# Optimization experiments

Hardware: AMD Instinct MI355X
Metric: run time of the kernel (lower is better)

The kernel has to match this reference:

```python
import jax, jax.numpy as jnp
import numpy as np

BN_EPS = 1e-5


def _tconv(X, w1, b1, w2, b2, w3, b3):
    # X: (B, T, N, C) -> conv over time with kernel (1, k), gated GLU-style
    Xp = X.transpose(0, 2, 1, 3)  # (B, N, T, C)
    def conv(w, b):
        return jax.lax.conv_general_dilated(
            Xp, w, (1, 1), 'VALID',
            dimension_numbers=('NHWC', 'HWIO', 'NHWC')) + b
    P = conv(w1, b1)
    Q = jax.nn.sigmoid(conv(w2, b2))
    R = conv(w3, b3)
    H = jax.nn.relu(P * Q + R)
    return H.transpose(0, 2, 1, 3)  # (B, T-k+1, N, Cout)


def _cheb(x, ei, W, b):
    # Batched ChebConv (sym norm, lambda_max=2 => L_hat = -D^-1/2 A D^-1/2)
    # x: (S, N, F), ei: (S, 2, E), W: (K, F, Fout)
    S, N, F = x.shape
    row, col = ei[:, 0], ei[:, 1]           # (S, E)
    ones = jnp.ones(ei.shape[-1], x.dtype)
    def norm_one(r, c):
        deg = jax.ops.segment_sum(ones, r, num_segments=N)
        dis = jnp.where(deg > 0, jax.lax.rsqrt(jnp.maximum(deg, 1.)), 0.)
        return -dis[r] * dis[c]
    w = jax.vmap(norm_one)(row, col)        # (S, E), constant wrt floats
    def prop(xs, r, c, ws):
        return jax.ops.segment_sum(ws[:, None] * xs[c], r, num_segments=N)
    propv = jax.vmap(prop)
    Tx = [x, propv(x, row, col, w)]
    for _ in range(W.shape[0] - 2):
        Tx.append(2. * propv(Tx[-1], row, col, w) - Tx[-2])
    return jnp.einsum('ksnf,kfo->sno', jnp.stack(Tx), W) + b


def _forward(X, tc1_w1, tc1_b1, tc1_w2, tc1_b2, tc1_w3, tc1_b3,
             cheb_w, cheb_b,
             tc2_w1, tc2_b1, tc2_w2, tc2_b2, tc2_w3, tc2_b3,
             bn_gamma, bn_beta, conv3_w, conv3_b, f1_w, f1_b, edge_index):
    T0 = _tconv(X, tc1_w1, tc1_b1, tc1_w2, tc1_b2, tc1_w3, tc1_b3)  # (B,38,N,H)
    B, Tt, N, H = T0.shape
    ei = edge_index[:, :Tt].reshape(B * Tt, 2, edge_index.shape[-1])
    G = _cheb(T0.reshape(B * Tt, N, H), ei, cheb_w, cheb_b)
    G = jax.nn.relu(G.reshape(B, Tt, N, H))
    T2 = _tconv(G, tc2_w1, tc2_b1, tc2_w2, tc2_b2, tc2_w3, tc2_b3)  # (B,36,N,Co)
    # BatchNorm2d over channel dim = num_nodes (training-mode batch stats)
    Tn = T2.transpose(0, 2, 1, 3)  # (B, N, T, C)
    mean = Tn.mean(axis=(0, 2, 3), keepdims=True)
    var = Tn.var(axis=(0, 2, 3), keepdims=True)
    Tn = (Tn - mean) * jax.lax.rsqrt(var + BN_EPS)
    Tn = Tn * bn_gamma[None, :, None, None] + bn_beta[None, :, None, None]
    Tb = Tn.transpose(0, 2, 1, 3)                 # (B, T, N, C)
    Tr = Tb.reshape(B, Tb.shape[1], -1)           # (B, T, N*C=3200)
    y = jax.lax.conv_general_dilated(
        Tr[:, None, :, :], conv3_w, (1, 1), 'VALID',
        dimension_numbers=('NCHW', 'OIHW', 'NCHW'))  # (B,128,T-2,1)
    y = y + conv3_b[None, :, None, None]
    y = y[:, :, :, 0]
    pooled = y.mean(axis=2)                        # AvgPool1d over full length
    return pooled @ f1_w + f1_b                    # (B, 3200)


def setup_inputs() -> dict:
    key = jax.random.key(0)
    ks = jax.random.split(key, 20)
    B, Tw, N, Cin, H, Co, E = 32, 40, 50, 2, 128, 64, 800
    KT, K = 3, 3
    s = 0.05
    d = {
        'X': jax.random.normal(ks[0], (B, Tw, N, Cin), jnp.float32),
        'edge_index': jax.random.randint(ks[1], (B, Tw, 2, E), 0, N),
        'tc1_w1': jax.random.normal(ks[2], (1, KT, Cin, H), jnp.float32) * s,
        'tc1_b1': jnp.zeros((H,), jnp.float32),
        'tc1_w2': jax.random.normal(ks[3], (1, KT, Cin, H), jnp.float32) * s,
        'tc1_b2': jnp.zeros((H,), jnp.float32),
        'tc1_w3': jax.random.normal(ks[4], (1, KT, Cin, H), jnp.float32) * s,
        'tc1_b3': jnp.zeros((H,), jnp.float32),
        'cheb_w': jax.random.normal(ks[5], (K, H, H), jnp.float32) * s,
        'cheb_b': jnp.zeros((H,), jnp.float32),
        'tc2_w1': jax.random.normal(ks[6], (1, KT, H, Co), jnp.float32) * s,
        'tc2_b1': jnp.zeros((Co,), jnp.float32),
        'tc2_w2': jax.random.normal(ks[7], (1, KT, H, Co), jnp.float32) * s,
        'tc2_b2': jnp.zeros((Co,), jnp.float32),
        'tc2_w3': jax.random.normal(ks[8], (1, KT, H, Co), jnp.float32) * s,
        'tc2_b3': jnp.zeros((Co,), jnp.float32),
        'bn_gamma': jnp.ones((N,), jnp.float32),
        'bn_beta': jnp.zeros((N,), jnp.float32),
        'conv3_w': jax.random.normal(ks[9], (128, 1, 3, N * Co), jnp.float32) * 0.01,
        'conv3_b': jnp.zeros((128,), jnp.float32),
        'f1_w': jax.random.normal(ks[10], (128, N * Co), jnp.float32) * s,
        'f1_b': jnp.zeros((N * Co,), jnp.float32),
    }
    return d


def reference(X, tc1_w1, tc1_b1, tc1_w2, tc1_b2, tc1_w3, tc1_b3,
              cheb_w, cheb_b,
              tc2_w1, tc2_b1, tc2_w2, tc2_b2, tc2_w3, tc2_b3,
              bn_gamma, bn_beta, conv3_w, conv3_b, f1_w, f1_b, edge_index):
    return _forward(X, tc1_w1, tc1_b1, tc1_w2, tc1_b2, tc1_w3, tc1_b3,
                    cheb_w, cheb_b,
                    tc2_w1, tc2_b1, tc2_w2, tc2_b2, tc2_w3, tc2_b3,
                    bn_gamma, bn_beta, conv3_w, conv3_b, f1_w, f1_b, edge_index)
```

## Files before the change

kernel.cpp:

```cpp
#include <hip/hip_runtime.h>
#include <hip/hip_bf16.h>

#define BB 32
#define TW 40
#define NN 50
#define HH 128
#define CO 64
#define EE 800
#define TT 38
#define TT2 36
#define TPOOL 34
#define NCO 3200
#define SS (BB*TT)
#define NPAD 64
#define RPAD (SS*NPAD)

#define PB_US ((size_t)RPAD * HH)
#define PB_BYTES (PB_US * 2)

typedef __attribute__((ext_vector_type(8))) short s16x8;
typedef __attribute__((ext_vector_type(16))) float f32x16;
typedef unsigned short us;

static __device__ __forceinline__ unsigned int f2bf_u(float x) {
    unsigned int u = __float_as_uint(x);
    return (u + 0x7fffu + ((u >> 16) & 1u)) >> 16;
}
static __device__ __forceinline__ float bfu2f(unsigned int h) {
    return __uint_as_float(h << 16);
}
static __device__ __forceinline__ size_t fragoff32(int m, int c) {
    return (size_t)(c >> 4) * 512 + ((c >> 3) & 1) * 256 + m * 8 + (c & 7);
}
#define MFMA(a, b, c) __builtin_amdgcn_mfma_f32_32x32x16_bf16((a), (b), (c), 0, 0, 0)

__global__ __launch_bounds__(256) void k_wprep(
    const float* __restrict__ cw,
    const float* __restrict__ tw1, const float* __restrict__ tw2, const float* __restrict__ tw3,
    us* __restrict__ VTh, us* __restrict__ VTl,
    us* __restrict__ WTh, us* __restrict__ WTl,
    float* __restrict__ pooled)
{
    int idx = blockIdx.x * 256 + threadIdx.x;
    float v; us *dh, *dl; int col, k;
    if (idx < 128 * 384) {
        col = idx / 384; k = idx % 384;
        if (k < 128)      v = cw[k * 128 + col] - cw[32768 + k * 128 + col];
        else if (k < 256) v = cw[16384 + (k - 128) * 128 + col];
        else              v = 2.f * cw[32768 + (k - 256) * 128 + col];
        dh = VTh; dl = VTl;
    } else if (idx < 128 * 384 + 192 * 384) {
        int i2 = idx - 128 * 384;
        col = i2 / 384; k = i2 % 384;
        int gg = col >> 6, o = col & 63;
        const float* src = (gg == 0) ? tw1 : (gg == 1) ? tw2 : tw3;
        v = src[k * 64 + o];
        dh = WTh; dl = WTl;
    } else {
        int z = idx - (128 * 384 + 192 * 384);
        if (z < 4096) pooled[z] = 0.f;
        return;
    }
    size_t off = ((size_t)((col >> 5) * 24 + (k >> 4)) * 64 + ((k >> 3) & 1) * 32 + (col & 31)) * 8
               + (k & 7);
    unsigned int h = f2bf_u(v);
    dh[off] = (us)h;
    dl[off] = (us)f2bf_u(v - bfu2f(h));
}

#define TAS 136
#define TBS 72
#define LMS 53
__global__ __launch_bounds__(256) void k_cheb(
    const int* __restrict__ EI, const float* __restrict__ X,
    const float* __restrict__ w1, const float* __restrict__ b1,
    const float* __restrict__ w2, const float* __restrict__ b2,
    const float* __restrict__ w3, const float* __restrict__ b3,
    const us* __restrict__ VTh, const us* __restrict__ VTl,
    const float* __restrict__ bias,
    us* __restrict__ Gh)
{
    __shared__ __align__(16) char smem[61440];
    us* TbA = (us*)smem;
    us* TbB = (us*)(smem + 17408);
    us* Pa  = (us*)(smem + 35840);
    float* Lm = (float*)(smem + 35840);
    us* LA  = (us*)(smem + 53248);
    float* Xs = (float*)(smem + 53248);
    int* deg  = (int*)(smem + 53248 + 1216);
    float* dis = (float*)(smem + 53248 + 1216 + 224);

    int g = blockIdx.x;
    int tid = threadIdx.x;
    int b = g / TT, t = g % TT;
    const int* row = EI + (size_t)(b * TW + t) * 2 * EE;
    const int* col = row + EE;

    {
        s16x8 zz = {0, 0, 0, 0, 0, 0, 0, 0};
        for (int i = tid; i < 2240; i += 256) ((s16x8*)smem)[i] = zz;
    }
    for (int i = tid; i < 52 * LMS; i += 256) Lm[i] = 0.f;
    for (int i = tid; i < 300; i += 256) Xs[i] = X[(size_t)(b * TW + t) * 100 + i];
    if (tid < NN) deg[tid] = 0;
    __syncthreads();

    {
        int c = tid & 127, nh = tid >> 7;
        float wr1[6], wr2[6], wr3[6];
#pragma unroll
        for (int q = 0; q < 6; q++) {
            wr1[q] = w1[q * HH + c];
            wr2[q] = w2[q * HH + c];
            wr3[q] = w3[q * HH + c];
        }
        float bv1 = b1[c], bv2 = b2[c], bv3 = b3[c];
        for (int n = nh; n < NN; n += 2) {
            float P = bv1, Q = bv2, R = bv3;
#pragma unroll
            for (int q = 0; q < 6; q++) {
                float x = Xs[(q >> 1) * 100 + n * 2 + (q & 1)];
                P += x * wr1[q]; Q += x * wr2[q]; R += x * wr3[q];
            }
            float sg = 1.f / (1.f + expf(-Q));
            float v = P * sg + R;
            v = v > 0.f ? v : 0.f;
            us h = (us)f2bf_u(v);
            TbA[n * TAS + c] = h;
            TbB[c * TBS + n] = h;
        }
    }
    __syncthreads();
    for (int e = tid; e < EE; e += 256) atomicAdd(&deg[row[e]], 1);
    __syncthreads();
    if (tid < NN) dis[tid] = deg[tid] > 0 ? rsqrtf((float)deg[tid]) : 0.f;
    __syncthreads();
    for (int e = tid; e < EE; e += 256) {
        int r = row[e], cc = col[e];
        atomicAdd(&Lm[r * LMS + cc], -dis[r] * dis[cc]);
    }
    __syncthreads();
    for (int ent = tid; ent < 512; ent += 256) {
        int lanee = ent & 63;
        int ks = (ent >> 6) & 3;
        int mt = ent >> 8;
        int m = mt * 32 + (lanee & 31);
        int kb = ks * 16 + (lanee >> 5) * 8;
        s16x8 v;
#pragma unroll
        for (int j = 0; j < 8; j++) {
            int k = kb + j;
            float lv = (m < NN && k < NN) ? Lm[m * LMS + k] : 0.f;
            v[j] = (short)f2bf_u(lv);
        }
        *(s16x8*)(LA + ent * 8) = v;
    }
    __syncthreads();

    int lane = tid & 63;
    int w = tid >> 6;
    int rg = w >> 1, fh = w & 1;
    int nl = lane & 31;
    int khalf = lane >> 5;
    size_t laneoff = (size_t)lane * 8;

    const us* vh0 = VTh + (size_t)(fh * 2) * 12288 + laneoff;
    const us* vh1 = VTh + (size_t)(fh * 2 + 1) * 12288 + laneoff;
    const us* vl0 = VTl + (size_t)(fh * 2) * 12288 + laneoff;
    const us* vl1 = VTl + (size_t)(fh * 2 + 1) * 12288 + laneoff;

    int mrowA = rg * 32 + nl;
    int kbb = khalf * 8;

    f32x16 gacc0, gacc1, d0, d1;
#pragma unroll
    for (int r = 0; r < 16; r++) { gacc0[r] = 0.f; gacc1[r] = 0.f; d0[r] = 0.f; d1[r] = 0.f; }

#pragma unroll
    for (int ks = 0; ks < 4; ks++) {
        s16x8 afr = *(const s16x8*)(LA + ((rg * 4 + ks) * 64 + lane) * 8);
        int kb = ks * 16 + kbb;
        s16x8 bf0 = *(const s16x8*)(TbB + (fh * 64 + nl) * TBS + kb);
        s16x8 bf1 = *(const s16x8*)(TbB + (fh * 64 + 32 + nl) * TBS + kb);
        d0 = MFMA(afr, bf0, d0);
        d1 = MFMA(afr, bf1, d1);
    }
#pragma unroll
    for (int ks = 0; ks < 8; ks++) {
        s16x8 ah = *(const s16x8*)(TbA + mrowA * TAS + ks * 16 + kbb);
        s16x8 bh0 = *(const s16x8*)(vh0 + ks * 512);
        s16x8 bl0 = *(const s16x8*)(vl0 + ks * 512);
        s16x8 bh1 = *(const s16x8*)(vh1 + ks * 512);
        s16x8 bl1 = *(const s16x8*)(vl1 + ks * 512);
        gacc0 = MFMA(ah, bh0, gacc0); gacc0 = MFMA(ah, bl0, gacc0);
        gacc1 = MFMA(ah, bh1, gacc1); gacc1 = MFMA(ah, bl1, gacc1);
    }
    __syncthreads();
#pragma unroll
    for (int r = 0; r < 16; r++) {
        int mrow = (r & 3) + 8 * (r >> 2) + 4 * khalf;
        int node = rg * 32 + mrow;
        int f0 = fh * 64 + nl, f1 = f0 + 32;
        us h0 = (us)f2bf_u(d0[r]);
        us h1 = (us)f2bf_u(d1[r]);
        Pa[node * TAS + f0] = h0;
        Pa[node * TAS + f1] = h1;
        TbB[f0 * TBS + node] = h0;
        TbB[f1 * TBS + node] = h1;
    }
    __syncthreads();

#pragma unroll
    for (int r = 0; r < 16; r++) { d0[r] = 0.f; d1[r] = 0.f; }
#pragma unroll
    for (int ks = 0; ks < 4; ks++) {
        s16x8 afr = *(const s16x8*)(LA + ((rg * 4 + ks) * 64 + lane) * 8);
        int kb = ks * 16 + kbb;
        s16x8 bf0 = *(const s16x8*)(TbB + (fh * 64 + nl) * TBS + kb);
        s16x8 bf1 = *(const s16x8*)(TbB + (fh * 64 + 32 + nl) * TBS + kb);
        d0 = MFMA(afr, bf0, d0);
        d1 = MFMA(afr, bf1, d1);
    }
#pragma unroll
    for (int ks = 0; ks < 8; ks++) {
        s16x8 ah = *(const s16x8*)(Pa + mrowA * TAS + ks * 16 + kbb);
        s16x8 bh0 = *(const s16x8*)(vh0 + (8 + ks) * 512);
        s16x8 bl0 = *(const s16x8*)(vl0 + (8 + ks) * 512);
        s16x8 bh1 = *(const s16x8*)(vh1 + (8 + ks) * 512);
        s16x8 bl1 = *(const s16x8*)(vl1 + (8 + ks) * 512);
        gacc0 = MFMA(ah, bh0, gacc0); gacc0 = MFMA(ah, bl0, gacc0);
        gacc1 = MFMA(ah, bh1, gacc1); gacc1 = MFMA(ah, bl1, gacc1);
    }
    __syncthreads();
#pragma unroll
    for (int r = 0; r < 16; r++) {
        int mrow = (r & 3) + 8 * (r >> 2) + 4 * khalf;
        int node = rg * 32 + mrow;
        int f0 = fh * 64 + nl, f1 = f0 + 32;
        Pa[node * TAS + f0] = (us)f2bf_u(d0[r]);
        Pa[node * TAS + f1] = (us)f2bf_u(d1[r]);
    }
    __syncthreads();
#pragma unroll
    for (int ks = 0; ks < 8; ks++) {
        s16x8 ah = *(const s16x8*)(Pa + mrowA * TAS + ks * 16 + kbb);
        s16x8 bh0 = *(const s16x8*)(vh0 + (16 + ks) * 512);
        s16x8 bl0 = *(const s16x8*)(vl0 + (16 + ks) * 512);
        s16x8 bh1 = *(const s16x8*)(vh1 + (16 + ks) * 512);
        s16x8 bl1 = *(const s16x8*)(vl1 + (16 + ks) * 512);
        gacc0 = MFMA(ah, bh0, gacc0); gacc0 = MFMA(ah, bl0, gacc0);
        gacc1 = MFMA(ah, bh1, gacc1); gacc1 = MFMA(ah, bl1, gacc1);
    }

    int c0 = fh * 64 + nl, c1 = c0 + 32;
    float bv0 = bias[c0], bv1 = bias[c1];
    size_t gb = (size_t)g * 8192 + (size_t)rg * 4096;
#pragma unroll
    for (int r = 0; r < 16; r++) {
        int mrow = (r & 3) + 8 * (r >> 2) + 4 * khalf;
        float v0 = gacc0[r] + bv0; v0 = v0 > 0.f ? v0 : 0.f;
        float v1 = gacc1[r] + bv1; v1 = v1 > 0.f ? v1 : 0.f;
        Gh[gb + fragoff32(mrow, c0)] = (us)f2bf_u(v0);
        Gh[gb + fragoff32(mrow, c1)] = (us)f2bf_u(v1);
    }
}

__global__ __launch_bounds__(128) void k_tc2(
    const us* __restrict__ Gh,
    const us* __restrict__ WTh, const us* __restrict__ WTl,
    const float* __restrict__ tb1, const float* __restrict__ tb2, const float* __restrict__ tb3,
    us* __restrict__ T2)
{
    int tid = threadIdx.x;
    int lane = tid & 63;
    int w = tid >> 6;
    int nl = lane & 31;
    size_t laneoff = (size_t)lane * 8;
    int i = blockIdx.x;
    int vb = (i & 7) * 288 + (i >> 3);
    int bt36 = vb >> 1, ntile = vb & 1;
    int b = bt36 / TT2, t = bt36 % TT2;

    const us* A[3];
#pragma unroll
    for (int k3 = 0; k3 < 3; k3++)
        A[k3] = Gh + (size_t)(b * TT + t + k3) * 8192 + (size_t)ntile * 4096 + laneoff;
    const us* Bh[3];
    const us* Bl[3];
#pragma unroll
    for (int g3 = 0; g3 < 3; g3++) {
        size_t cb = (size_t)(g3 * 2 + w) * 12288 + laneoff;
        Bh[g3] = WTh + cb;
        Bl[g3] = WTl + cb;
    }

    f32x16 aP, aQ, aR;
#pragma unroll
    for (int r = 0; r < 16; r++) { aP[r] = 0.f; aQ[r] = 0.f; aR[r] = 0.f; }

#pragma unroll
    for (int k3 = 0; k3 < 3; k3++) {
#pragma unroll
        for (int ls = 0; ls < 8; ls++) {
            int offB = (k3 * 8 + ls) * 512;
            s16x8 a0 = *(const s16x8*)(A[k3] + ls * 512);
            s16x8 ph = *(const s16x8*)(Bh[0] + offB);
            s16x8 pl = *(const s16x8*)(Bl[0] + offB);
            s16x8 qh = *(const s16x8*)(Bh[1] + offB);
            s16x8 ql = *(const s16x8*)(Bl[1] + offB);
            s16x8 rh = *(const s16x8*)(Bh[2] + offB);
            s16x8 rl = *(const s16x8*)(Bl[2] + offB);
            aP = MFMA(a0, ph, aP); aP = MFMA(a0, pl, aP);
            aQ = MFMA(a0, qh, aQ); aQ = MFMA(a0, ql, aQ);
            aR = MFMA(a0, rh, aR); aR = MFMA(a0, rl, aR);
        }
    }

    int o = w * 32 + nl;
    float bP = tb1[o], bQ = tb2[o], bR = tb3[o];
    int rbase = (lane >> 5) * 4;
#pragma unroll
    for (int r = 0; r < 16; r++) {
        int m = (r & 3) + 8 * (r >> 2) + rbase;
        int node = ntile * 32 + m;
        if (node < NN) {
            float P = aP[r] + bP, Q = aQ[r] + bQ, R = aR[r] + bR;
            float sg = 1.f / (1.f + expf(-Q));
            float v = P * sg + R;
            v = v > 0.f ? v : 0.f;
            T2[((size_t)bt36 * NN + node) * CO + o] = (us)f2bf_u(v);
        }
    }
}

__global__ __launch_bounds__(256) void k_bnpart(const us* __restrict__ T2, float* __restrict__ partial)
{
    int n = blockIdx.x >> 3, c = blockIdx.x & 7;
    int tid = threadIdx.x;
    float s = 0.f, ss = 0.f;
    for (int i = tid; i < 144 * 64; i += 256) {
        int bt = c * 144 + (i >> 6), o = i & 63;
        float v = bfu2f(T2[((size_t)bt * NN + n) * CO + o]);
        s += v; ss += v * v;
    }
    for (int off = 32; off > 0; off >>= 1) { s += __shfl_down(s, off, 64); ss += __shfl_down(ss, off, 64); }
    __shared__ float rs[4], rss[4];
    int lane = tid & 63, wv = tid >> 6;
    if (lane == 0) { rs[wv] = s; rss[wv] = ss; }
    __syncthreads();
    if (tid == 0) {
        partial[n * 8 + c] = rs[0] + rs[1] + rs[2] + rs[3];
        partial[400 + n * 8 + c] = rss[0] + rss[1] + rss[2] + rss[3];
    }
}

__global__ __launch_bounds__(64) void k_bnfin(const float* __restrict__ partial, float* __restrict__ stats)
{
    int n = threadIdx.x;
    if (n < NN) {
        float s = 0.f, ss = 0.f;
#pragma unroll
        for (int c = 0; c < 8; c++) { s += partial[n * 8 + c]; ss += partial[400 + n * 8 + c]; }
        const float inv = 1.f / (float)(BB * TT2 * CO);
        float m = s * inv;
        float var = ss * inv - m * m;
        stats[n] = m;
        stats[64 + n] = rsqrtf(var + 1e-5f);
    }
}

__global__ __launch_bounds__(256) void k_upool(
    const us* __restrict__ T2, const float* __restrict__ stats,
    const float* __restrict__ gamma, const float* __restrict__ beta,
    const float* __restrict__ W3, float* __restrict__ pooled)
{
    __shared__ __align__(16) float Ul[48 * 36 + 32];
    __shared__ float Ws[128 * 9];
    int blk = blockIdx.x;
    int jc = blk * 16;
    int n0 = jc >> 6;
    int tid = threadIdx.x;
    float mn = stats[n0], is = stats[64 + n0];
    float sc = is * gamma[n0];
    float off = (float)TPOOL * beta[n0] - (float)TPOOL * mn * sc;

    {
        int j = tid & 15, b0 = tid >> 4;
#pragma unroll
        for (int bp = 0; bp < 2; bp++) {
            int bb = b0 + 16 * bp;
            const us* p = T2 + (size_t)bb * TT2 * NCO + jc + j;
            float s0 = 0.f;
            for (int t = 0; t < TPOOL; t++) s0 += bfu2f(p[(size_t)t * NCO]);
            float s1 = s0 - bfu2f(p[0]) + bfu2f(p[(size_t)34 * NCO]);
            float s2 = s1 - bfu2f(p[(size_t)1 * NCO]) + bfu2f(p[(size_t)35 * NCO]);
            Ul[(0 * 16 + j) * 36 + bb] = s0 * sc + off;
            Ul[(1 * 16 + j) * 36 + bb] = s1 * sc + off;
            Ul[(2 * 16 + j) * 36 + bb] = s2 * sc + off;
        }
    }
    __syncthreads();

    int o = tid & 127, bq = tid >> 7;
    float acc[16];
#pragma unroll
    for (int i = 0; i < 16; i++) acc[i] = 0.f;

    for (int kjc = 0; kjc < 48; kjc += 8) {
        __syncthreads();
#pragma unroll
        for (int p4 = 0; p4 < 4; p4++) {
            int idx = p4 * 256 + tid;
            int oo = idx >> 3, q = idx & 7;
            int kj = kjc + q;
            Ws[oo * 9 + q] = W3[(size_t)oo * 9600 + (kj >> 4) * 3200 + jc + (kj & 15)];
        }
        __syncthreads();
#pragma unroll
        for (int q = 0; q < 8; q++) {
            float wv = Ws[o * 9 + q];
            const float* up = &Ul[(kjc + q) * 36 + bq * 16];
#pragma unroll
            for (int i4 = 0; i4 < 4; i4++) {
                float4 u = *(const float4*)(up + i4 * 4);
                acc[i4 * 4 + 0] += wv * u.x;
                acc[i4 * 4 + 1] += wv * u.y;
                acc[i4 * 4 + 2] += wv * u.z;
                acc[i4 * 4 + 3] += wv * u.w;
            }
        }
    }
#pragma unroll
    for (int i = 0; i < 16; i++)
        atomicAdd(&pooled[(size_t)(bq * 16 + i) * 128 + o], acc[i]);
}

__global__ __launch_bounds__(256) void k_final(
    const float* __restrict__ pooled, const float* __restrict__ b3c,
    const float* __restrict__ f1w, const float* __restrict__ f1b,
    float* __restrict__ out)
{
    __shared__ float pb[32 * 129];
    int tid = threadIdx.x;
    const float inv = 1.f / (float)TPOOL;
    for (int i = tid; i < 4096; i += 256) {
        int b = i >> 7, o = i & 127;
        pb[b * 129 + o] = pooled[b * 128 + o] * inv + b3c[o];
    }
    __syncthreads();
    int q = blockIdx.x * 8 + (tid & 7);
    int b = tid >> 3;
    float acc = f1b[q];
    const float* wq = f1w + q;
    const float* pbb = pb + b * 129;
#pragma unroll 4
    for (int o = 0; o < 128; o++) acc += pbb[o] * wq[(size_t)o * NCO];
    out[(size_t)b * NCO + q] = acc;
}

extern "C" void kernel_launch(void* const* d_in, const int* in_sizes, int n_in,
                              void* d_out, int out_size, void* d_ws, size_t ws_size,
                              hipStream_t stream)
{
    const float* X       = (const float*)d_in[0];
    const int*   EI      = (const int*)d_in[1];
    const float* tc1_w1  = (const float*)d_in[2];
    const float* tc1_b1  = (const float*)d_in[3];
    const float* tc1_w2  = (const float*)d_in[4];
    const float* tc1_b2  = (const float*)d_in[5];
    const float* tc1_w3  = (const float*)d_in[6];
    const float* tc1_b3  = (const float*)d_in[7];
    const float* cheb_w  = (const float*)d_in[8];
    const float* cheb_b  = (const float*)d_in[9];
    const float* tc2_w1  = (const float*)d_in[10];
    const float* tc2_b1  = (const float*)d_in[11];
    const float* tc2_w2  = (const float*)d_in[12];
    const float* tc2_b2  = (const float*)d_in[13];
    const float* tc2_w3  = (const float*)d_in[14];
    const float* tc2_b3  = (const float*)d_in[15];
    const float* bn_g    = (const float*)d_in[16];
    const float* bn_b    = (const float*)d_in[17];
    const float* conv3_w = (const float*)d_in[18];
    const float* conv3_b = (const float*)d_in[19];
    const float* f1_w    = (const float*)d_in[20];
    const float* f1_b    = (const float*)d_in[21];

    char* base = (char*)d_ws;
    us*    Gh     = (us*)base;
    us*    T2     = (us*)(base + PB_BYTES);
    float* pooled = (float*)(base + PB_BYTES + 7372800);
    float* stats  = (float*)(base + PB_BYTES + 7389184);
    float* partial= (float*)(base + PB_BYTES + 7389696);
    us*    VTh    = (us*)(base + PB_BYTES + 7392896);
    us*    VTl    = VTh + 49152;
    us*    WTh    = VTl + 49152;
    us*    WTl    = WTh + 73728;

    k_wprep<<<496, 256, 0, stream>>>(cheb_w, tc2_w1, tc2_w2, tc2_w3, VTh, VTl, WTh, WTl, pooled);
    k_cheb<<<SS, 256, 0, stream>>>(EI, X, tc1_w1, tc1_b1, tc1_w2, tc1_b2, tc1_w3, tc1_b3,
                                   VTh, VTl, cheb_b, Gh);
    k_tc2<<<2304, 128, 0, stream>>>(Gh, WTh, WTl, tc2_b1, tc2_b2, tc2_b3, T2);
    k_bnpart<<<NN * 8, 256, 0, stream>>>(T2, partial);
    k_bnfin<<<1, 64, 0, stream>>>(partial, stats);
    k_upool<<<200, 256, 0, stream>>>(T2, stats, bn_g, bn_b, conv3_w, pooled);
    k_final<<<NCO / 8, 256, 0, stream>>>(pooled, conv3_b, f1_w, f1_b, (float*)d_out);
}
```

Measured before the change: 234.6 us.

## Merge BN finalize into upool, coalesce bnpart with atomics, shrink cheb LDS

The batch-norm partial reduction now walks T2 contiguously, with each block covering 200 rows of 64 channels. It accumulates per-node sums through wave reductions, LDS atomics and global atomics into a zeroed buffer. The separate finalize kernel is removed, and upool computes the mean and inverse std itself, which saves a launch and avoids strided reads. In k_cheb, the Pa buffer is aliased onto TbA and the Lm padding is reduced, shrinking shared memory from 61440 to 54272 bytes so more blocks can be resident per CU. The float atomic accumulation makes the statistics order-nondeterministic.

```diff
diff --git a/kernel.cpp b/kernel.cpp
--- a/kernel.cpp
+++ b/kernel.cpp
@@ -39,7 +39,7 @@
     const float* __restrict__ tw1, const float* __restrict__ tw2, const float* __restrict__ tw3,
     us* __restrict__ VTh, us* __restrict__ VTl,
     us* __restrict__ WTh, us* __restrict__ WTl,
-    float* __restrict__ pooled)
+    float* __restrict__ pooled, float* __restrict__ gpart)
 {
     int idx = blockIdx.x * 256 + threadIdx.x;
     float v; us *dh, *dl; int col, k;
@@ -59,6 +59,7 @@
     } else {
         int z = idx - (128 * 384 + 192 * 384);
         if (z < 4096) pooled[z] = 0.f;
+        else if (z < 4224) gpart[z - 4096] = 0.f;
         return;
     }
     size_t off = ((size_t)((col >> 5) * 24 + (k >> 4)) * 64 + ((k >> 3) & 1) * 32 + (col & 31)) * 8
@@ -70,7 +71,7 @@
 
 #define TAS 136
 #define TBS 72
-#define LMS 53
+#define LMS 51
 __global__ __launch_bounds__(256) void k_cheb(
     const int* __restrict__ EI, const float* __restrict__ X,
     const float* __restrict__ w1, const float* __restrict__ b1,
@@ -80,15 +81,14 @@
     const float* __restrict__ bias,
     us* __restrict__ Gh)
 {
-    __shared__ __align__(16) char smem[61440];
+    __shared__ __align__(16) char smem[54272];
     us* TbA = (us*)smem;
     us* TbB = (us*)(smem + 17408);
-    us* Pa  = (us*)(smem + 35840);
-    float* Lm = (float*)(smem + 35840);
-    us* LA  = (us*)(smem + 53248);
-    float* Xs = (float*)(smem + 53248);
-    int* deg  = (int*)(smem + 53248 + 1216);
-    float* dis = (float*)(smem + 53248 + 1216 + 224);
+    us* LA  = (us*)(smem + 35840);
+    float* Lm = (float*)(smem + 44032);
+    float* Xs = (float*)(smem + 35840);
+    int* deg  = (int*)(smem + 35840 + 1216);
+    float* dis = (float*)(smem + 35840 + 1216 + 224);
 
     int g = blockIdx.x;
     int tid = threadIdx.x;
@@ -100,7 +100,7 @@
         s16x8 zz = {0, 0, 0, 0, 0, 0, 0, 0};
         for (int i = tid; i < 2240; i += 256) ((s16x8*)smem)[i] = zz;
     }
-    for (int i = tid; i < 52 * LMS; i += 256) Lm[i] = 0.f;
+    for (int i = tid; i < 50 * LMS; i += 256) Lm[i] = 0.f;
     for (int i = tid; i < 300; i += 256) Xs[i] = X[(size_t)(b * TW + t) * 100 + i];
     if (tid < NN) deg[tid] = 0;
     __syncthreads();
@@ -203,8 +203,8 @@
         int f0 = fh * 64 + nl, f1 = f0 + 32;
         us h0 = (us)f2bf_u(d0[r]);
         us h1 = (us)f2bf_u(d1[r]);
-        Pa[node * TAS + f0] = h0;
-        Pa[node * TAS + f1] = h1;
+        TbA[node * TAS + f0] = h0;
+        TbA[node * TAS + f1] = h1;
         TbB[f0 * TBS + node] = h0;
         TbB[f1 * TBS + node] = h1;
     }
@@ -223,7 +223,7 @@
     }
 #pragma unroll
     for (int ks = 0; ks < 8; ks++) {
-        s16x8 ah = *(const s16x8*)(Pa + mrowA * TAS + ks * 16 + kbb);
+        s16x8 ah = *(const s16x8*)(TbA + mrowA * TAS + ks * 16 + kbb);
         s16x8 bh0 = *(const s16x8*)(vh0 + (8 + ks) * 512);
         s16x8 bl0 = *(const s16x8*)(vl0 + (8 + ks) * 512);
         s16x8 bh1 = *(const s16x8*)(vh1 + (8 + ks) * 512);
@@ -237,13 +237,13 @@
         int mrow = (r & 3) + 8 * (r >> 2) + 4 * khalf;
         int node = rg * 32 + mrow;
         int f0 = fh * 64 + nl, f1 = f0 + 32;
-        Pa[node * TAS + f0] = (us)f2bf_u(d0[r]);
-        Pa[node * TAS + f1] = (us)f2bf_u(d1[r]);
+        TbA[node * TAS + f0] = (us)f2bf_u(d0[r]);
+        TbA[node * TAS + f1] = (us)f2bf_u(d1[r]);
     }
     __syncthreads();
 #pragma unroll
     for (int ks = 0; ks < 8; ks++) {
-        s16x8 ah = *(const s16x8*)(Pa + mrowA * TAS + ks * 16 + kbb);
+        s16x8 ah = *(const s16x8*)(TbA + mrowA * TAS + ks * 16 + kbb);
         s16x8 bh0 = *(const s16x8*)(vh0 + (16 + ks) * 512);
         s16x8 bl0 = *(const s16x8*)(vl0 + (16 + ks) * 512);
         s16x8 bh1 = *(const s16x8*)(vh1 + (16 + ks) * 512);
@@ -333,44 +333,35 @@
     }
 }
 
-__global__ __launch_bounds__(256) void k_bnpart(const us* __restrict__ T2, float* __restrict__ partial)
-{
-    int n = blockIdx.x >> 3, c = blockIdx.x & 7;
+__global__ __launch_bounds__(256) void k_bnpart(const us* __restrict__ T2, float* __restrict__ gpart)
+{
+    __shared__ float ns[52], nss[52];
     int tid = threadIdx.x;
-    float s = 0.f, ss = 0.f;
-    for (int i = tid; i < 144 * 64; i += 256) {
-        int bt = c * 144 + (i >> 6), o = i & 63;
-        float v = bfu2f(T2[((size_t)bt * NN + n) * CO + o]);
-        s += v; ss += v * v;
-    }
-    for (int off = 32; off > 0; off >>= 1) { s += __shfl_down(s, off, 64); ss += __shfl_down(ss, off, 64); }
-    __shared__ float rs[4], rss[4];
-    int lane = tid & 63, wv = tid >> 6;
-    if (lane == 0) { rs[wv] = s; rss[wv] = ss; }
-    __syncthreads();
-    if (tid == 0) {
-        partial[n * 8 + c] = rs[0] + rs[1] + rs[2] + rs[3];
-        partial[400 + n * 8 + c] = rss[0] + rss[1] + rss[2] + rss[3];
-    }
-}
-
-__global__ __launch_bounds__(64) void k_bnfin(const float* __restrict__ partial, float* __restrict__ stats)
-{
-    int n = threadIdx.x;
-    if (n < NN) {
-        float s = 0.f, ss = 0.f;
-#pragma unroll
-        for (int c = 0; c < 8; c++) { s += partial[n * 8 + c]; ss += partial[400 + n * 8 + c]; }
-        const float inv = 1.f / (float)(BB * TT2 * CO);
-        float m = s * inv;
-        float var = ss * inv - m * m;
-        stats[n] = m;
-        stats[64 + n] = rsqrtf(var + 1e-5f);
+    int lane = tid & 63, w = tid >> 6;
+    if (tid < NN) { ns[tid] = 0.f; nss[tid] = 0.f; }
+    __syncthreads();
+    const us* base = T2 + (size_t)blockIdx.x * 12800;
+    for (int it = 0; it < 50; it++) {
+        int idx = it * 256 + w * 64 + lane;
+        float v = bfu2f(base[idx]);
+        int node = ((it * 4 + w)) % 50;
+        float s = v, ss = v * v;
+#pragma unroll
+        for (int off = 32; off > 0; off >>= 1) {
+            s += __shfl_down(s, off, 64);
+            ss += __shfl_down(ss, off, 64);
+        }
+        if (lane == 0) { atomicAdd(&ns[node], s); atomicAdd(&nss[node], ss); }
+    }
+    __syncthreads();
+    if (tid < NN) {
+        atomicAdd(&gpart[tid], ns[tid]);
+        atomicAdd(&gpart[64 + tid], nss[tid]);
     }
 }
 
 __global__ __launch_bounds__(256) void k_upool(
-    const us* __restrict__ T2, const float* __restrict__ stats,
+    const us* __restrict__ T2, const float* __restrict__ gpart,
     const float* __restrict__ gamma, const float* __restrict__ beta,
     const float* __restrict__ W3, float* __restrict__ pooled)
 {
@@ -380,7 +371,10 @@
     int jc = blk * 16;
     int n0 = jc >> 6;
     int tid = threadIdx.x;
-    float mn = stats[n0], is = stats[64 + n0];
+    const float inv = 1.f / (float)(BB * TT2 * CO);
+    float mn = gpart[n0] * inv;
+    float var = gpart[64 + n0] * inv - mn * mn;
+    float is = rsqrtf(var + 1e-5f);
     float sc = is * gamma[n0];
     float off = (float)TPOOL * beta[n0] - (float)TPOOL * mn * sc;
 
@@ -489,19 +483,17 @@
     us*    Gh     = (us*)base;
     us*    T2     = (us*)(base + PB_BYTES);
     float* pooled = (float*)(base + PB_BYTES + 7372800);
-    float* stats  = (float*)(base + PB_BYTES + 7389184);
-    float* partial= (float*)(base + PB_BYTES + 7389696);
-    us*    VTh    = (us*)(base + PB_BYTES + 7392896);
+    float* gpart  = (float*)(base + PB_BYTES + 7389184);
+    us*    VTh    = (us*)(base + PB_BYTES + 7389696);
     us*    VTl    = VTh + 49152;
     us*    WTh    = VTl + 49152;
     us*    WTl    = WTh + 73728;
 
-    k_wprep<<<496, 256, 0, stream>>>(cheb_w, tc2_w1, tc2_w2, tc2_w3, VTh, VTl, WTh, WTl, pooled);
+    k_wprep<<<497, 256, 0, stream>>>(cheb_w, tc2_w1, tc2_w2, tc2_w3, VTh, VTl, WTh, WTl, pooled, gpart);
     k_cheb<<<SS, 256, 0, stream>>>(EI, X, tc1_w1, tc1_b1, tc1_w2, tc1_b2, tc1_w3, tc1_b3,
                                    VTh, VTl, cheb_b, Gh);
     k_tc2<<<2304, 128, 0, stream>>>(Gh, WTh, WTl, tc2_b1, tc2_b2, tc2_b3, T2);
-    k_bnpart<<<NN * 8, 256, 0, stream>>>(T2, partial);
-    k_bnfin<<<1, 64, 0, stream>>>(partial, stats);
-    k_upool<<<200, 256, 0, stream>>>(T2, stats, bn_g, bn_b, conv3_w, pooled);
+    k_bnpart<<<288, 256, 0, stream>>>(T2, gpart);
+    k_upool<<<200, 256, 0, stream>>>(T2, gpart, bn_g, bn_b, conv3_w, pooled);
     k_final<<<NCO / 8, 256, 0, stream>>>(pooled, conv3_b, f1_w, f1_b, (float*)d_out);
 }
```

New measurement: 254.4 us. 1.08x slower.
